# Performance work log

Measured on AMD Instinct MI355X. Metric: run time of the kernel, lower is better.

## Reference

```python
import jax, jax.numpy as jnp
import numpy as np
import math

B, QLEN, KLEN = 8, 128, 1024
KDIM = QDIM = ADIM = ODIM = 512
HM, HC = 4, 4            # monotonic / chunkwise heads
CHUNK = 4                # chunkwise attention window
EPS = 1e-6
SHARPENING = 1.0
NEG_INF = float(np.finfo(np.float32).min)


def moving_sum(x, back, forward):
    """Windowed sum over last axis: out[k] = sum_{j=k-back}^{k+forward} x[j].
    Equivalent to the conv1d-with-ones-filter moving_sum in the torch code."""
    K = x.shape[-1]
    xp = jnp.pad(x, [(0, 0)] * (x.ndim - 1) + [(back, forward)])
    cs = jnp.cumsum(xp, axis=-1)
    L = back + forward + 1
    upper = jax.lax.slice_in_dim(cs, L - 1, L - 1 + K, axis=-1)
    lower = jnp.concatenate([jnp.zeros_like(cs[..., :1]),
                             jax.lax.slice_in_dim(cs, 0, K - 1, axis=-1)], axis=-1)
    return upper - lower


def safe_cumprod(x, eps):
    """exp(exclusive_cumsum(log(clip(x, eps, 1)))) along last axis."""
    logx = jnp.log(jnp.clip(x, eps, 1.0))
    excl = jnp.concatenate([jnp.zeros_like(logx[..., :1]),
                            jnp.cumsum(logx, axis=-1)[..., :-1]], axis=-1)
    return jnp.exp(excl)


def _heads(x, w, b, h):
    y = x @ w + b                                   # [B, L, ADIM]
    bs, L, _ = y.shape
    return y.reshape(bs, L, h, -1).transpose(0, 2, 1, 3)  # [B, h, L, d_k]


def setup_inputs() -> dict:
    key = jax.random.key(0)
    ks = jax.random.split(key, 16)
    s = 0.02
    f32 = jnp.float32
    return {
        "key_x": jax.random.normal(ks[0], (B, KLEN, KDIM), f32),
        "query_x": jax.random.normal(ks[1], (B, QLEN, QDIM), f32),
        "mask": jnp.ones((B, QLEN, KLEN), jnp.int32),
        "wk_m": jax.random.normal(ks[2], (KDIM, ADIM), f32) * s,
        "bk_m": jnp.zeros((ADIM,), f32),
        "wq_m": jax.random.normal(ks[3], (QDIM, ADIM), f32) * s,
        "bq_m": jnp.zeros((ADIM,), f32),
        "r": jnp.asarray(-4.0, f32),
        "wk_c": jax.random.normal(ks[4], (KDIM, ADIM), f32) * s,
        "bk_c": jnp.zeros((ADIM,), f32),
        "wq_c": jax.random.normal(ks[5], (QDIM, ADIM), f32) * s,
        "bq_c": jnp.zeros((ADIM,), f32),
        "wv": jax.random.normal(ks[6], (KDIM, ADIM), f32) * s,
        "bv": jnp.zeros((ADIM,), f32),
        "wo": jax.random.normal(ks[7], (ADIM, ODIM), f32) * s,
        "bo": jnp.zeros((ODIM,), f32),
    }


def reference(key_x, query_x, mask, wk_m, bk_m, wq_m, bq_m, r,
              wk_c, bk_c, wq_c, bq_c, wv, bv, wo, bo):
    scale = math.sqrt(ADIM)
    m = (mask[:, None] > 0)                                    # [B,1,Q,K]

    # ---- monotonic energy (scaled_dot + offset r) ----
    km = _heads(key_x, wk_m, bk_m, HM)                         # [B,HM,K,dk]
    qm = _heads(query_x, wq_m, bq_m, HM)                       # [B,HM,Q,dk]
    e_mono = jnp.einsum('bhqd,bhkd->bhqk', qm, km) / scale + r
    e_mono = jnp.where(m, e_mono, NEG_INF)

    # ---- monotonic alpha via safe_cumprod + per-step cumsum recurrence ----
    p_choose = jax.nn.sigmoid(e_mono)                          # [B,HM,Q,K]
    cp = safe_cumprod(1.0 - p_choose, EPS)                     # [B,HM,Q,K]
    aw0 = jnp.zeros((B, HM, KLEN), e_mono.dtype).at[..., 0].set(1.0)

    def step(aw_prev, pc):
        p_i, cp_i = pc                                         # [B,HM,K]
        aw = p_i * cp_i * jnp.cumsum(aw_prev / jnp.maximum(cp_i, EPS), axis=-1)
        return aw, aw

    _, alpha = jax.lax.scan(step, aw0,
                            (p_choose.transpose(2, 0, 1, 3),
                             cp.transpose(2, 0, 1, 3)))
    alpha = alpha.transpose(1, 2, 0, 3)                        # [B,HM,Q,K]

    # ---- chunkwise energy ----
    kc = _heads(key_x, wk_c, bk_c, HC)
    qc = _heads(query_x, wq_c, bq_c, HC)
    e_chunk = jnp.einsum('bhqd,bhkd->bhqk', qc, kc) / scale
    e_chunk = jnp.where(m, e_chunk, NEG_INF)

    # ---- efficient chunkwise attention (clipped-logit trick) ----
    e = e_chunk - jnp.max(e_chunk, axis=-1, keepdims=True)
    sexp = jnp.maximum(jnp.exp(e), 1e-5)[:, None]              # [B,1,HC,Q,K]
    denom = moving_sum(sexp, CHUNK - 1, 0)                     # [B,1,HC,Q,K]
    beta = sexp * moving_sum(alpha[:, :, None] * SHARPENING / denom,
                             0, CHUNK - 1)                     # [B,HM,HC,Q,K]
    beta = beta.reshape(B, HM * HC, QLEN, KLEN)

    # ---- context + output projection ----
    v = (key_x @ wv + bv).reshape(B, KLEN, HM * HC, ADIM // (HM * HC))
    cv = jnp.einsum('bhqk,bkhd->bqhd', beta, v).reshape(B, QLEN, ADIM)
    return cv @ wo + bo
```

## Files before the change

### kernel.cpp

```cpp
#include <hip/hip_runtime.h>
#include <hip/hip_bf16.h>


#define NEG_INF (-3.402823466e38f)
#define EPS_MOCHA 1e-6f
#define INV_SCALE 0.04419417382415922f

typedef _Float16 half8 __attribute__((ext_vector_type(8)));
typedef _Float16 half4v __attribute__((ext_vector_type(4)));
typedef float f32x4 __attribute__((ext_vector_type(4)));

#define WAITBAR(N) asm volatile("s_waitcnt vmcnt(" #N ") lgkmcnt(0)\n\ts_barrier" ::: "memory")

__device__ __forceinline__ float frcp(float x) { return __builtin_amdgcn_rcpf(x); }

__device__ __forceinline__ float wave_incl_scan(float x)
{
    int v;
    v = __builtin_amdgcn_update_dpp(0, __builtin_bit_cast(int, x), 0x111, 0xF, 0xF, false);
    x += __builtin_bit_cast(float, v);
    v = __builtin_amdgcn_update_dpp(0, __builtin_bit_cast(int, x), 0x112, 0xF, 0xF, false);
    x += __builtin_bit_cast(float, v);
    v = __builtin_amdgcn_update_dpp(0, __builtin_bit_cast(int, x), 0x114, 0xF, 0xF, false);
    x += __builtin_bit_cast(float, v);
    v = __builtin_amdgcn_update_dpp(0, __builtin_bit_cast(int, x), 0x118, 0xF, 0xF, false);
    x += __builtin_bit_cast(float, v);
    v = __builtin_amdgcn_update_dpp(0, __builtin_bit_cast(int, x), 0x142, 0xA, 0xF, false);
    x += __builtin_bit_cast(float, v);
    v = __builtin_amdgcn_update_dpp(0, __builtin_bit_cast(int, x), 0x143, 0xC, 0xF, false);
    x += __builtin_bit_cast(float, v);
    return x;
}

__device__ __forceinline__ half8 cvt8(float4 a, float4 b)
{
    half8 h = {(_Float16)a.x, (_Float16)a.y, (_Float16)a.z, (_Float16)a.w,
               (_Float16)b.x, (_Float16)b.y, (_Float16)b.z, (_Float16)b.w};
    return h;
}

__global__ __launch_bounds__(256) void prep_all(
    const float* __restrict__ wk_m, const float* __restrict__ wk_c,
    const float* __restrict__ wv, const float* __restrict__ wq_m,
    const float* __restrict__ wq_c, const float* __restrict__ wo,
    const float* __restrict__ key_x, const float* __restrict__ query_x,
    _Float16* __restrict__ Wt5, _Float16* __restrict__ Wt_wo,
    _Float16* __restrict__ X16)
{
    __shared__ float T[64][65];
    const int bid = blockIdx.x;
    const int t = threadIdx.x;
    if (bid < 384) {
        const int z = bid >> 6, w = bid & 63;
        const float* W = (z == 0) ? wk_m : (z == 1) ? wk_c : (z == 2) ? wv
                       : (z == 3) ? wq_m : (z == 4) ? wq_c : wo;
        _Float16* O = (z < 5) ? (Wt5 + (size_t)z * 262144) : Wt_wo;
        const int n0 = (w & 7) * 64, k0 = (w >> 3) * 64;
        const int rr = t >> 4, cc = (t & 15) * 4;
#pragma unroll
        for (int r = 0; r < 4; ++r) {
            int k = r * 16 + rr;
            float4 v = *(const float4*)(W + (size_t)(k0 + k) * 512 + n0 + cc);
            T[k][cc + 0] = v.x; T[k][cc + 1] = v.y;
            T[k][cc + 2] = v.z; T[k][cc + 3] = v.w;
        }
        __syncthreads();
        const int nn = t >> 2, kc = (t & 3) * 16;
        _Float16 tmp[16];
#pragma unroll
        for (int i = 0; i < 16; ++i) tmp[i] = (_Float16)T[kc + i][nn];
        _Float16* Op = O + (size_t)(n0 + nn) * 512 + k0 + kc;
        *(half8*)(Op)     = *(half8*)&tmp[0];
        *(half8*)(Op + 8) = *(half8*)&tmp[8];
    } else {
        const size_t KELEMS = (size_t)8192 * 512;
        size_t o = ((size_t)(bid - 384) * 256 + t) * 8;
        const float* s = (o < KELEMS) ? (key_x + o) : (query_x + (o - KELEMS));
        float4 a = *(const float4*)s;
        float4 b = *(const float4*)(s + 4);
        *(half8*)(X16 + o) = cvt8(a, b);
    }
}

__device__ __forceinline__ void stage16(const _Float16* src, _Float16* dst)
{
    __builtin_amdgcn_global_load_lds(
        (const __attribute__((address_space(1))) void*)src,
        (__attribute__((address_space(3))) void*)dst, 16, 0, 0);
}

template <int NSTEPS>
__device__ __forceinline__ void gemm8_f16(
    const _Float16* __restrict__ Abase, const _Float16* __restrict__ Bbase,
    _Float16* As, _Float16* Bs, f32x4 acc[4][2])
{
    const int tid = threadIdx.x;
    const int lane = tid & 63, wave = tid >> 6;
    const int wm = wave >> 2, wn = wave & 3;
    const int col = lane & 15, quad = lane >> 4;
    const int r0 = tid >> 2, seg = tid & 3;

    const _Float16* Ag = Abase + (size_t)r0 * 512 + seg * 8;
    const _Float16* Bg = Bbase + (size_t)r0 * 512 + seg * 8;

    stage16(Ag, As + tid * 8);
    stage16(Bg, Bs + tid * 8);
    if (NSTEPS > 1) {
        stage16(Ag + 32, As + 4096 + tid * 8);
        stage16(Bg + 32, Bs + 4096 + tid * 8);
        WAITBAR(2);
    } else {
        WAITBAR(0);
    }

#pragma unroll
    for (int ks = 0; ks < NSTEPS; ++ks) {
        const int cur = ks % 3;
        if (ks + 2 < NSTEPS) {
            const int s2 = (ks + 2) % 3;
            stage16(Ag + (ks + 2) * 32, As + s2 * 4096 + tid * 8);
            stage16(Bg + (ks + 2) * 32, Bs + s2 * 4096 + tid * 8);
        }
        const _Float16* Afr = As + cur * 4096 + (size_t)(wm * 64 + col) * 32 + quad * 8;
        const _Float16* Bfr = Bs + cur * 4096 + (size_t)(wn * 32 + col) * 32 + quad * 8;
        half8 a[4], b[2];
#pragma unroll
        for (int t = 0; t < 4; ++t) a[t] = *(const half8*)(Afr + (size_t)t * 16 * 32);
#pragma unroll
        for (int t = 0; t < 2; ++t) b[t] = *(const half8*)(Bfr + (size_t)t * 16 * 32);
#pragma unroll
        for (int mt = 0; mt < 4; ++mt)
#pragma unroll
            for (int nt = 0; nt < 2; ++nt)
                acc[mt][nt] = __builtin_amdgcn_mfma_f32_16x16x32_f16(
                    a[mt], b[nt], acc[mt][nt], 0, 0, 0);
        if (ks + 2 < NSTEPS)      WAITBAR(2);
        else if (ks + 1 < NSTEPS) WAITBAR(0);
    }
}

__device__ __forceinline__ void proj_epilogue8(
    f32x4 acc[4][2], const float* __restrict__ bias, void* __restrict__ Cv,
    int m0, int n0, int f16o)
{
    const int tid = threadIdx.x;
    const int lane = tid & 63, wave = tid >> 6;
    const int wm = wave >> 2, wn = wave & 3;
    const int col = lane & 15, quad = lane >> 4;
    float bnt[2];
#pragma unroll
    for (int nt = 0; nt < 2; ++nt)
        bnt[nt] = bias[n0 + wn * 32 + nt * 16 + col];
#pragma unroll
    for (int mt = 0; mt < 4; ++mt) {
        const int rowb = m0 + wm * 64 + mt * 16 + quad * 4;
#pragma unroll
        for (int nt = 0; nt < 2; ++nt) {
            const int cc = n0 + wn * 32 + nt * 16 + col;
#pragma unroll
            for (int r = 0; r < 4; ++r) {
                float v = acc[mt][nt][r] + bnt[nt];
                if (f16o)
                    ((_Float16*)Cv)[(size_t)(rowb + r) * 512 + cc] = (_Float16)v;
                else
                    ((float*)Cv)[(size_t)(rowb + r) * 512 + cc] = v;
            }
        }
    }
}

__global__ __launch_bounds__(512, 8) void mfma_proj5(
    const _Float16* __restrict__ X16, const _Float16* __restrict__ Wt5,
    const float* __restrict__ b0, void* __restrict__ C0,
    const float* __restrict__ b1, void* __restrict__ C1,
    const float* __restrict__ b2, void* __restrict__ C2,
    const float* __restrict__ b3, void* __restrict__ C3,
    const float* __restrict__ b4, void* __restrict__ C4)
{
    __shared__ _Float16 As[12288];
    __shared__ _Float16 Bs[12288];
    const int bid = (blockIdx.x & 7) * 104 + (blockIdx.x >> 3);
    int g, mblk, nblk;
    if (bid < 768) {
        g = bid >> 8; mblk = (bid & 255) >> 2; nblk = bid & 3;
    } else {
        const int t = bid - 768;
        g = 3 + (t >> 5); mblk = (t & 31) >> 2; nblk = t & 3;
    }
    const bool qry = g >= 3;
    const _Float16* A = X16 + (qry ? (size_t)8192 * 512 : 0);
    const _Float16* Wt = Wt5 + (size_t)g * 262144;
    const float* bias = (g == 0) ? b0 : (g == 1) ? b1 : (g == 2) ? b2
                      : (g == 3) ? b3 : b4;
    void* Cv = (g == 0) ? C0 : (g == 1) ? C1 : (g == 2) ? C2
             : (g == 3) ? C3 : C4;
    const int m0 = mblk * 128, n0 = nblk * 128;

    f32x4 acc[4][2];
#pragma unroll
    for (int mt = 0; mt < 4; ++mt)
#pragma unroll
        for (int nt = 0; nt < 2; ++nt) acc[mt][nt] = (f32x4)0.f;
    gemm8_f16<16>(A + (size_t)m0 * 512, Wt + (size_t)n0 * 512, As, Bs, acc);
    proj_epilogue8(acc, bias, Cv, m0, n0, 1);
}

__global__ __launch_bounds__(512, 4) void mfma_proj_out(
    const _Float16* __restrict__ A16, const _Float16* __restrict__ Wt,
    const float* __restrict__ bias, float* __restrict__ C)
{
    __shared__ _Float16 As[12288];
    __shared__ _Float16 Bs[12288];
    const int m0 = blockIdx.x * 128, n0 = blockIdx.y * 128;
    f32x4 acc[4][2];
#pragma unroll
    for (int mt = 0; mt < 4; ++mt)
#pragma unroll
        for (int nt = 0; nt < 2; ++nt) acc[mt][nt] = (f32x4)0.f;
    gemm8_f16<16>(A16 + (size_t)m0 * 512, Wt + (size_t)n0 * 512, As, Bs, acc);
    proj_epilogue8(acc, bias, C, m0, n0, 0);
}

__global__ __launch_bounds__(512, 4) void energy_mfma(
    const _Float16* __restrict__ Qm, const _Float16* __restrict__ Km,
    const _Float16* __restrict__ Qc, const _Float16* __restrict__ Kc,
    const int* __restrict__ mask, float* __restrict__ e_mono,
    _Float16* __restrict__ e_chunk16, const float* __restrict__ r_ptr)
{
    __shared__ _Float16 As[12288];
    __shared__ _Float16 Bs[12288];
    const int tid = threadIdx.x;
    const int lane = tid & 63, wave = tid >> 6;
    const int wm = wave >> 2, wn = wave & 3;
    const int col = lane & 15, quad = lane >> 4;
    const int kt0 = blockIdx.x * 128;
    const int h = blockIdx.y;
    const int b = blockIdx.z;
    const float rv = r_ptr[0];
    const int r0 = tid >> 2, seg = tid & 3;

    const _Float16* Am0 = Qm + (size_t)(b * 128) * 512 + h * 128 + (size_t)r0 * 512 + seg * 8;
    const _Float16* Ac0 = Qc + (size_t)(b * 128) * 512 + h * 128 + (size_t)r0 * 512 + seg * 8;
    const _Float16* Bm0 = Km + (size_t)(b * 1024 + kt0) * 512 + h * 128 + (size_t)r0 * 512 + seg * 8;
    const _Float16* Bc0 = Kc + (size_t)(b * 1024 + kt0) * 512 + h * 128 + (size_t)r0 * 512 + seg * 8;
#define EGA(s) (((s) < 4 ? Am0 : Ac0) + ((s) & 3) * 32)
#define EGB(s) (((s) < 4 ? Bm0 : Bc0) + ((s) & 3) * 32)

    f32x4 accM[4][2], accC[4][2];
#pragma unroll
    for (int mt = 0; mt < 4; ++mt)
#pragma unroll
        for (int nt = 0; nt < 2; ++nt) { accM[mt][nt] = (f32x4)0.f; accC[mt][nt] = (f32x4)0.f; }

#pragma unroll
    for (int s = 0; s < 2; ++s) {
        stage16(EGA(s), As + s * 4096 + tid * 8);
        stage16(EGB(s), Bs + s * 4096 + tid * 8);
    }
    WAITBAR(2);

#pragma unroll
    for (int ks = 0; ks < 8; ++ks) {
        const int cur = ks % 3;
        if (ks + 2 < 8) {
            const int s2 = (ks + 2) % 3;
            stage16(EGA(ks + 2), As + s2 * 4096 + tid * 8);
            stage16(EGB(ks + 2), Bs + s2 * 4096 + tid * 8);
        }
        const _Float16* Afr = As + cur * 4096 + (size_t)(wm * 64 + col) * 32 + quad * 8;
        const _Float16* Bfr = Bs + cur * 4096 + (size_t)(wn * 32 + col) * 32 + quad * 8;
        half8 a[4], bf[2];
#pragma unroll
        for (int t = 0; t < 4; ++t) a[t]  = *(const half8*)(Afr + (size_t)t * 16 * 32);
#pragma unroll
        for (int t = 0; t < 2; ++t) bf[t] = *(const half8*)(Bfr + (size_t)t * 16 * 32);
        if (ks < 4) {
#pragma unroll
            for (int mt = 0; mt < 4; ++mt)
#pragma unroll
                for (int nt = 0; nt < 2; ++nt)
                    accM[mt][nt] = __builtin_amdgcn_mfma_f32_16x16x32_f16(a[mt], bf[nt], accM[mt][nt], 0, 0, 0);
        } else {
#pragma unroll
            for (int mt = 0; mt < 4; ++mt)
#pragma unroll
                for (int nt = 0; nt < 2; ++nt)
                    accC[mt][nt] = __builtin_amdgcn_mfma_f32_16x16x32_f16(a[mt], bf[nt], accC[mt][nt], 0, 0, 0);
        }
        if (ks + 2 < 8)      WAITBAR(2);
        else if (ks + 1 < 8) WAITBAR(0);
    }
#undef EGA
#undef EGB

#pragma unroll
    for (int mt = 0; mt < 4; ++mt) {
        const int qb = wm * 64 + mt * 16 + quad * 4;
#pragma unroll
        for (int nt = 0; nt < 2; ++nt) {
            const int kc = kt0 + wn * 32 + nt * 16 + col;
#pragma unroll
            for (int r = 0; r < 4; ++r) {
                const int q = qb + r;
                const int mv = mask[((size_t)b * 128 + q) * 1024 + kc];
                const size_t oi = (((size_t)b * 4 + h) * 128 + q) * 1024 + kc;
                float vm = accM[mt][nt][r] * INV_SCALE + rv;
                e_mono[oi] = mv ? vm : NEG_INF;
                float vc = accC[mt][nt][r] * INV_SCALE;
                e_chunk16[oi] = (_Float16)(mv ? vc : NEG_INF);
            }
        }
    }
}

__device__ __forceinline__ void transcend_row(
    const float* __restrict__ Erow, int lane, float o_pcp[16], float o_inv[16])
{
    const float* E = Erow + lane * 16;
    float e[16];
    *(float4*)&e[0]  = *(const float4*)(E);
    *(float4*)&e[4]  = *(const float4*)(E + 4);
    *(float4*)&e[8]  = *(const float4*)(E + 8);
    *(float4*)&e[12] = *(const float4*)(E + 12);

    float p[16], l[16];
#pragma unroll
    for (int i = 0; i < 16; ++i) {
        p[i] = frcp(1.f + __expf(-e[i]));
        l[i] = __logf(fmaxf(1.f - p[i], EPS_MOCHA));
    }
    float incl[16];
    incl[0] = l[0];
#pragma unroll
    for (int i = 1; i < 16; ++i) incl[i] = incl[i - 1] + l[i];
    float total = incl[15];
    float x = wave_incl_scan(total);
    float base = x - total;
#pragma unroll
    for (int i = 0; i < 16; ++i) {
        float cl = base + (i ? incl[i - 1] : 0.f);
        float cp = __expf(cl);
        o_pcp[i] = p[i] * cp;
        o_inv[i] = frcp(fmaxf(cp, EPS_MOCHA));
    }
}

#define SW2(k) ((k) + ((k) >> 4))

__global__ __launch_bounds__(512) void alpha_pre(
    const float* __restrict__ e_mono, float* __restrict__ G,
    float* __restrict__ pcp)
{
    __shared__ float pshare[8][1088];
    const int tid = threadIdx.x;
    const int lane = tid & 63;
    const int wid = tid >> 6;
    const int row = blockIdx.x * 8 + wid;
    const int q = row & 127;

    float pq[16], iq[16];
    transcend_row(e_mono + (size_t)row * 1024, lane, pq, iq);

    float* P = pcp + (size_t)row * 1024 + lane * 16;
    *(float4*)(P)      = *(float4*)&pq[0];
    *(float4*)(P + 4)  = *(float4*)&pq[4];
    *(float4*)(P + 8)  = *(float4*)&pq[8];
    *(float4*)(P + 12) = *(float4*)&pq[12];

#pragma unroll
    for (int i = 0; i < 16; ++i)
        pshare[wid][SW2(lane * 16 + i)] = pq[i];
    __syncthreads();

    float g[16];
    if (q == 0) {
#pragma unroll
        for (int i = 0; i < 16; ++i) g[i] = 0.f;
        if (lane == 0) g[0] = iq[0];
    } else if (wid > 0) {
#pragma unroll
        for (int i = 0; i < 16; ++i)
            g[i] = pshare[wid - 1][SW2(lane * 16 + i)] * iq[i];
    } else {
        float pm[16], im[16];
        transcend_row(e_mono + (size_t)(row - 1) * 1024, lane, pm, im);
#pragma unroll
        for (int i = 0; i < 16; ++i) g[i] = pm[i] * iq[i];
    }
    float* Gp = G + (size_t)row * 1024 + lane * 16;
    *(float4*)(Gp)      = *(float4*)&g[0];
    *(float4*)(Gp + 4)  = *(float4*)&g[4];
    *(float4*)(Gp + 8)  = *(float4*)&g[8];
    *(float4*)(Gp + 12) = *(float4*)&g[12];
}

__global__ __launch_bounds__(64, 1) void alpha_scan(
    const float* __restrict__ G, const float* __restrict__ pcp,
    float* __restrict__ alpha)
{
    const int lane = threadIdx.x;
    const int bh = blockIdx.x;
    const float* Gp = G + (size_t)bh * 131072 + lane * 16;
    const float* Pp = pcp + (size_t)bh * 131072 + lane * 16;
    float* Ap = alpha + (size_t)bh * 131072 + lane * 16;

    float bg[8][16], bp[8][16];
#pragma unroll
    for (int s = 0; s < 8; ++s) {
        const float* Gq = Gp + (size_t)s * 1024;
        const float* Pq = Pp + (size_t)s * 1024;
        *(float4*)&bg[s][0]  = *(const float4*)(Gq);
        *(float4*)&bg[s][4]  = *(const float4*)(Gq + 4);
        *(float4*)&bg[s][8]  = *(const float4*)(Gq + 8);
        *(float4*)&bg[s][12] = *(const float4*)(Gq + 12);
        *(float4*)&bp[s][0]  = *(const float4*)(Pq);
        *(float4*)&bp[s][4]  = *(const float4*)(Pq + 4);
        *(float4*)&bp[s][8]  = *(const float4*)(Pq + 8);
        *(float4*)&bp[s][12] = *(const float4*)(Pq + 12);
    }

    float Sv[16];
#pragma unroll
    for (int i = 0; i < 16; ++i) Sv[i] = 1.f;

    for (int q8 = 0; q8 < 128; q8 += 8) {
#pragma unroll
        for (int s = 0; s < 8; ++s) {
            const int q = q8 + s;
            float g[16], pv[16];
#pragma unroll
            for (int i = 0; i < 16; ++i) { g[i] = bg[s][i]; pv[i] = bp[s][i]; }
            if (q + 8 < 128) {
                const float* Gq = Gp + (size_t)(q + 8) * 1024;
                const float* Pq = Pp + (size_t)(q + 8) * 1024;
                *(float4*)&bg[s][0]  = *(const float4*)(Gq);
                *(float4*)&bg[s][4]  = *(const float4*)(Gq + 4);
                *(float4*)&bg[s][8]  = *(const float4*)(Gq + 8);
                *(float4*)&bg[s][12] = *(const float4*)(Gq + 12);
                *(float4*)&bp[s][0]  = *(const float4*)(Pq);
                *(float4*)&bp[s][4]  = *(const float4*)(Pq + 4);
                *(float4*)&bp[s][8]  = *(const float4*)(Pq + 8);
                *(float4*)&bp[s][12] = *(const float4*)(Pq + 12);
            }

            float incl[16];
            incl[0] = g[0] * Sv[0];
#pragma unroll
            for (int i = 1; i < 16; ++i)
                incl[i] = fmaf(g[i], Sv[i], incl[i - 1]);
            float total = incl[15];
            float x = wave_incl_scan(total);
            float base = x - total;
#pragma unroll
            for (int i = 0; i < 16; ++i) Sv[i] = base + incl[i];

            float av[16];
#pragma unroll
            for (int i = 0; i < 16; ++i) av[i] = pv[i] * Sv[i];
            float* Aq = Ap + (size_t)q * 1024;
            *(float4*)(Aq)      = *(float4*)&av[0];
            *(float4*)(Aq + 4)  = *(float4*)&av[4];
            *(float4*)(Aq + 8)  = *(float4*)&av[8];
            *(float4*)(Aq + 12) = *(float4*)&av[12];
        }
    }
}

__global__ __launch_bounds__(256) void beta_kernel(
    const _Float16* __restrict__ e_chunk16, const float* __restrict__ alpha,
    _Float16* __restrict__ beta)
{
    __shared__ float red[4];
    __shared__ float edge_sx[4][4];
    __shared__ float edge_t[4][4][4];
    const int q = blockIdx.x, b = blockIdx.y;
    const int tid = threadIdx.x;
    const int lane = tid & 63, wid = tid >> 6;
    const int k4 = tid * 4;

    float av[4][4];
#pragma unroll
    for (int hm = 0; hm < 4; ++hm) {
        const size_t off = (((size_t)b * 4 + hm) * 128 + q) * 1024 + k4;
        float4 a = *(const float4*)(alpha + off);
        av[hm][0] = a.x; av[hm][1] = a.y; av[hm][2] = a.z; av[hm][3] = a.w;
    }

    for (int hc = 0; hc < 4; ++hc) {
        half4v ev = *(const half4v*)(e_chunk16 + (((size_t)b * 4 + hc) * 128 + q) * 1024 + k4);
        float e[4] = {(float)ev[0], (float)ev[1], (float)ev[2], (float)ev[3]};

        float mx = fmaxf(fmaxf(e[0], e[1]), fmaxf(e[2], e[3]));
#pragma unroll
        for (int off = 32; off >= 1; off >>= 1)
            mx = fmaxf(mx, __shfl_xor(mx, off, 64));
        if (lane == 0) red[wid] = mx;
        __syncthreads();
        mx = fmaxf(fmaxf(red[0], red[1]), fmaxf(red[2], red[3]));

        float sx[4];
#pragma unroll
        for (int i = 0; i < 4; ++i)
            sx[i] = fmaxf(__expf(e[i] - mx), 1e-5f);
        if (lane == 63) {
            edge_sx[wid][0] = sx[0]; edge_sx[wid][1] = sx[1];
            edge_sx[wid][2] = sx[2]; edge_sx[wid][3] = sx[3];
        }
        __syncthreads();

        float p1 = __shfl_up(sx[3], 1, 64);
        float p2 = __shfl_up(sx[2], 1, 64);
        float p3 = __shfl_up(sx[1], 1, 64);
        if (lane == 0) {
            if (wid > 0) {
                p1 = edge_sx[wid - 1][3];
                p2 = edge_sx[wid - 1][2];
                p3 = edge_sx[wid - 1][1];
            } else {
                p1 = 0.f; p2 = 0.f; p3 = 0.f;
            }
        }
        float den[4];
        den[0] = sx[0] + p1 + p2 + p3;
        den[1] = sx[1] + sx[0] + p1 + p2;
        den[2] = sx[2] + sx[1] + sx[0] + p1;
        den[3] = sx[3] + sx[2] + sx[1] + sx[0];
        float rd[4];
#pragma unroll
        for (int i = 0; i < 4; ++i) rd[i] = frcp(den[i]);

        float t[4][4];
#pragma unroll
        for (int hm = 0; hm < 4; ++hm)
#pragma unroll
            for (int i = 0; i < 4; ++i)
                t[hm][i] = av[hm][i] * rd[i];
        if (lane == 0) {
#pragma unroll
            for (int hm = 0; hm < 4; ++hm) {
                edge_t[wid][hm][0] = t[hm][0]; edge_t[wid][hm][1] = t[hm][1];
                edge_t[wid][hm][2] = t[hm][2]; edge_t[wid][hm][3] = t[hm][3];
            }
        }
        __syncthreads();

#pragma unroll
        for (int hm = 0; hm < 4; ++hm) {
            float n1 = __shfl_down(t[hm][0], 1, 64);
            float n2 = __shfl_down(t[hm][1], 1, 64);
            float n3 = __shfl_down(t[hm][2], 1, 64);
            if (lane == 63) {
                if (wid < 3) {
                    n1 = edge_t[wid + 1][hm][0];
                    n2 = edge_t[wid + 1][hm][1];
                    n3 = edge_t[wid + 1][hm][2];
                } else {
                    n1 = 0.f; n2 = 0.f; n3 = 0.f;
                }
            }
            float o0 = sx[0] * (t[hm][0] + t[hm][1] + t[hm][2] + t[hm][3]);
            float o1 = sx[1] * (t[hm][1] + t[hm][2] + t[hm][3] + n1);
            float o2 = sx[2] * (t[hm][2] + t[hm][3] + n1 + n2);
            float o3 = sx[3] * (t[hm][3] + n1 + n2 + n3);
            _Float16* Brow = beta + (((size_t)b * 16 + hm * 4 + hc) * 128 + q) * 1024;
            half4v hv = {(_Float16)o0, (_Float16)o1, (_Float16)o2, (_Float16)o3};
            *(half4v*)(Brow + k4) = hv;
        }
    }
}

__global__ __launch_bounds__(256) void context_kernel(
    const _Float16* __restrict__ beta, const _Float16* __restrict__ V16,
    _Float16* __restrict__ cv16)
{
    __shared__ float bS[128][64];
    __shared__ float vS[128][32];
    const int qh = blockIdx.x, h = blockIdx.y, b = blockIdx.z;
    const int tid = threadIdx.x;
    const int ty = tid >> 3, tx = tid & 7;
    const int q0 = qh * 64;

    const _Float16* Bbase = beta + (((size_t)b * 16 + h) * 128 + q0) * 1024;
    const _Float16* Vbase = V16 + (size_t)b * 1024 * 512 + h * 32;

    float acc[2][4];
#pragma unroll
    for (int i = 0; i < 2; ++i)
#pragma unroll
        for (int j = 0; j < 4; ++j) acc[i][j] = 0.f;

    for (int k0 = 0; k0 < 1024; k0 += 128) {
        {
            int r = tid >> 2, c = tid & 3;
#pragma unroll
            for (int s = 0; s < 4; ++s) {
                half8 v = *(const half8*)(Bbase + (size_t)r * 1024 + k0 + s * 32 + c * 8);
#pragma unroll
                for (int j = 0; j < 8; ++j) bS[s * 32 + c * 8 + j][r] = (float)v[j];
            }
        }
        {
            int kk = tid >> 3, c = tid & 7;
#pragma unroll
            for (int s = 0; s < 4; ++s) {
                half4v v = *(const half4v*)(Vbase + (size_t)(k0 + s * 32 + kk) * 512 + c * 4);
                float4 f = {(float)v[0], (float)v[1], (float)v[2], (float)v[3]};
                *(float4*)&vS[s * 32 + kk][c * 4] = f;
            }
        }
        __syncthreads();
#pragma unroll 8
        for (int kk = 0; kk < 128; ++kk) {
            float a0 = bS[kk][ty * 2], a1 = bS[kk][ty * 2 + 1];
            float bb[4];
            *(float4*)bb = *(const float4*)&vS[kk][tx * 4];
#pragma unroll
            for (int j = 0; j < 4; ++j) {
                acc[0][j] = fmaf(a0, bb[j], acc[0][j]);
                acc[1][j] = fmaf(a1, bb[j], acc[1][j]);
            }
        }
        __syncthreads();
    }
#pragma unroll
    for (int i = 0; i < 2; ++i) {
        _Float16* Cp = cv16 + ((size_t)b * 128 + q0 + ty * 2 + i) * 512 + h * 32 + tx * 4;
        half4v hv = {(_Float16)acc[i][0], (_Float16)acc[i][1],
                     (_Float16)acc[i][2], (_Float16)acc[i][3]};
        *(half4v*)Cp = hv;
    }
}

extern "C" void kernel_launch(void* const* d_in, const int* in_sizes, int n_in,
                              void* d_out, int out_size, void* d_ws, size_t ws_size,
                              hipStream_t stream)
{
    const float* key_x   = (const float*)d_in[0];
    const float* query_x = (const float*)d_in[1];
    const int*   mask    = (const int*)d_in[2];
    const float* wk_m = (const float*)d_in[3];
    const float* bk_m = (const float*)d_in[4];
    const float* wq_m = (const float*)d_in[5];
    const float* bq_m = (const float*)d_in[6];
    const float* r    = (const float*)d_in[7];
    const float* wk_c = (const float*)d_in[8];
    const float* bk_c = (const float*)d_in[9];
    const float* wq_c = (const float*)d_in[10];
    const float* bq_c = (const float*)d_in[11];
    const float* wv   = (const float*)d_in[12];
    const float* bv   = (const float*)d_in[13];
    const float* wo   = (const float*)d_in[14];
    const float* bo   = (const float*)d_in[15];
    float* out = (float*)d_out;

    float* ws = (float*)d_ws;
    _Float16* hws = (_Float16*)d_ws;
    const size_t MEGF = 1024 * 1024;
    _Float16* Km16  = hws;
    _Float16* Kc16  = hws + 4 * MEGF;
    _Float16* Qm16  = hws + 8 * MEGF;
    _Float16* Qc16  = hws + 8 * MEGF + 524288;
    _Float16* X16   = hws + 16 * MEGF;
    float* e_mono  = ws + 11 * MEGF;
    _Float16* e_chunk16 = hws + 34 * MEGF;
    _Float16* V16  = hws + 38 * MEGF;
    float* G       = ws;
    float* pcp     = ws + 4 * MEGF;
    float* alpha   = ws + 23 * MEGF;
    _Float16* beta16 = hws + 16 * MEGF;
    _Float16* Wt5   = hws + 54 * MEGF;
    _Float16* Wt_wo = hws + 54 * MEGF + 5 * 262144;
    _Float16* cv16  = hws + 55 * MEGF + MEGF / 2;

    prep_all<<<dim3(2688), 256, 0, stream>>>(
        wk_m, wk_c, wv, wq_m, wq_c, wo, key_x, query_x, Wt5, Wt_wo, X16);
    mfma_proj5<<<dim3(832), 512, 0, stream>>>(
        X16, Wt5, bk_m, Km16, bk_c, Kc16, bv, V16, bq_m, Qm16, bq_c, Qc16);
    energy_mfma<<<dim3(8, 4, 8), 512, 0, stream>>>(
        Qm16, Km16, Qc16, Kc16, mask, e_mono, e_chunk16, r);
    alpha_pre<<<dim3(512), 512, 0, stream>>>(e_mono, G, pcp);
    alpha_scan<<<dim3(32), 64, 0, stream>>>(G, pcp, alpha);
    beta_kernel<<<dim3(128, 8), 256, 0, stream>>>(e_chunk16, alpha, beta16);
    context_kernel<<<dim3(2, 16, 8), 256, 0, stream>>>(beta16, V16, cv16);
    mfma_proj_out<<<dim3(8, 4), 512, 0, stream>>>(cv16, Wt_wo, bo, out);
}
```

Before: 255.8 us.

## Split alpha scan across four waves with LDS carry exchange per row

The alpha_scan kernel now uses 256 threads per (batch, head) block instead of a single wave. Each thread owns 4 keys instead of 16, and wave totals are combined through a double-buffered shared-memory carry with a barrier every query step. This shortens each thread's serial inner chain and spreads the loads over more lanes. The cost is 128 block barriers and some LDS traffic per block, and the grid stays at only 32 blocks.

```diff
diff --git a/kernel.cpp b/kernel.cpp
--- a/kernel.cpp
+++ b/kernel.cpp
@@ -11,6 +11,7 @@
 typedef float f32x4 __attribute__((ext_vector_type(4)));
 
 #define WAITBAR(N) asm volatile("s_waitcnt vmcnt(" #N ") lgkmcnt(0)\n\ts_barrier" ::: "memory")
+#define BARLG() asm volatile("s_waitcnt lgkmcnt(0)\n\ts_barrier" ::: "memory")
 
 __device__ __forceinline__ float frcp(float x) { return __builtin_amdgcn_rcpf(x); }
 
@@ -394,75 +395,54 @@
     *(float4*)(Gp + 12) = *(float4*)&g[12];
 }
 
-__global__ __launch_bounds__(64, 1) void alpha_scan(
+__global__ __launch_bounds__(256) void alpha_scan(
     const float* __restrict__ G, const float* __restrict__ pcp,
     float* __restrict__ alpha)
 {
-    const int lane = threadIdx.x;
+    __shared__ float carry[2][4];
+    const int tid = threadIdx.x;
+    const int lane = tid & 63, wid = tid >> 6;
     const int bh = blockIdx.x;
-    const float* Gp = G + (size_t)bh * 131072 + lane * 16;
-    const float* Pp = pcp + (size_t)bh * 131072 + lane * 16;
-    float* Ap = alpha + (size_t)bh * 131072 + lane * 16;
-
-    float bg[8][16], bp[8][16];
-#pragma unroll
-    for (int s = 0; s < 8; ++s) {
-        const float* Gq = Gp + (size_t)s * 1024;
-        const float* Pq = Pp + (size_t)s * 1024;
-        *(float4*)&bg[s][0]  = *(const float4*)(Gq);
-        *(float4*)&bg[s][4]  = *(const float4*)(Gq + 4);
-        *(float4*)&bg[s][8]  = *(const float4*)(Gq + 8);
-        *(float4*)&bg[s][12] = *(const float4*)(Gq + 12);
-        *(float4*)&bp[s][0]  = *(const float4*)(Pq);
-        *(float4*)&bp[s][4]  = *(const float4*)(Pq + 4);
-        *(float4*)&bp[s][8]  = *(const float4*)(Pq + 8);
-        *(float4*)&bp[s][12] = *(const float4*)(Pq + 12);
-    }
-
-    float Sv[16];
-#pragma unroll
-    for (int i = 0; i < 16; ++i) Sv[i] = 1.f;
-
-    for (int q8 = 0; q8 < 128; q8 += 8) {
-#pragma unroll
-        for (int s = 0; s < 8; ++s) {
-            const int q = q8 + s;
-            float g[16], pv[16];
-#pragma unroll
-            for (int i = 0; i < 16; ++i) { g[i] = bg[s][i]; pv[i] = bp[s][i]; }
-            if (q + 8 < 128) {
-                const float* Gq = Gp + (size_t)(q + 8) * 1024;
-                const float* Pq = Pp + (size_t)(q + 8) * 1024;
-                *(float4*)&bg[s][0]  = *(const float4*)(Gq);
-                *(float4*)&bg[s][4]  = *(const float4*)(Gq + 4);
-                *(float4*)&bg[s][8]  = *(const float4*)(Gq + 8);
-                *(float4*)&bg[s][12] = *(const float4*)(Gq + 12);
-                *(float4*)&bp[s][0]  = *(const float4*)(Pq);
-                *(float4*)&bp[s][4]  = *(const float4*)(Pq + 4);
-                *(float4*)&bp[s][8]  = *(const float4*)(Pq + 8);
-                *(float4*)&bp[s][12] = *(const float4*)(Pq + 12);
-            }
-
-            float incl[16];
-            incl[0] = g[0] * Sv[0];
-#pragma unroll
-            for (int i = 1; i < 16; ++i)
-                incl[i] = fmaf(g[i], Sv[i], incl[i - 1]);
-            float total = incl[15];
-            float x = wave_incl_scan(total);
-            float base = x - total;
-#pragma unroll
-            for (int i = 0; i < 16; ++i) Sv[i] = base + incl[i];
-
-            float av[16];
-#pragma unroll
-            for (int i = 0; i < 16; ++i) av[i] = pv[i] * Sv[i];
-            float* Aq = Ap + (size_t)q * 1024;
-            *(float4*)(Aq)      = *(float4*)&av[0];
-            *(float4*)(Aq + 4)  = *(float4*)&av[4];
-            *(float4*)(Aq + 8)  = *(float4*)&av[8];
-            *(float4*)(Aq + 12) = *(float4*)&av[12];
-        }
+    const float* Gp = G + (size_t)bh * 131072 + tid * 4;
+    const float* Pp = pcp + (size_t)bh * 131072 + tid * 4;
+    float* Ap = alpha + (size_t)bh * 131072 + tid * 4;
+
+    float4 bg[4], bp[4];
+#pragma unroll
+    for (int s = 0; s < 4; ++s) {
+        bg[s] = *(const float4*)(Gp + (size_t)s * 1024);
+        bp[s] = *(const float4*)(Pp + (size_t)s * 1024);
+    }
+
+    float Sv[4] = {1.f, 1.f, 1.f, 1.f};
+
+    for (int q = 0; q < 128; ++q) {
+        const int s = q & 3;
+        float g[4] = {bg[s].x, bg[s].y, bg[s].z, bg[s].w};
+        float p[4] = {bp[s].x, bp[s].y, bp[s].z, bp[s].w};
+        if (q + 4 < 128) {
+            bg[s] = *(const float4*)(Gp + (size_t)(q + 4) * 1024);
+            bp[s] = *(const float4*)(Pp + (size_t)(q + 4) * 1024);
+        }
+        float incl[4];
+        incl[0] = g[0] * Sv[0];
+        incl[1] = fmaf(g[1], Sv[1], incl[0]);
+        incl[2] = fmaf(g[2], Sv[2], incl[1]);
+        incl[3] = fmaf(g[3], Sv[3], incl[2]);
+        float t = incl[3];
+        float x = wave_incl_scan(t);
+        float base = x - t;
+        if (lane == 63) carry[q & 1][wid] = x;
+        BARLG();
+        float pre = 0.f;
+        if (wid > 0) pre += carry[q & 1][0];
+        if (wid > 1) pre += carry[q & 1][1];
+        if (wid > 2) pre += carry[q & 1][2];
+        float baseAll = pre + base;
+#pragma unroll
+        for (int i = 0; i < 4; ++i) Sv[i] = baseAll + incl[i];
+        float4 av = {p[0] * Sv[0], p[1] * Sv[1], p[2] * Sv[2], p[3] * Sv[3]};
+        *(float4*)(Ap + (size_t)q * 1024) = av;
     }
 }
 
@@ -679,7 +659,7 @@
     energy_mfma<<<dim3(8, 4, 8), 512, 0, stream>>>(
         Qm16, Km16, Qc16, Kc16, mask, e_mono, e_chunk16, r);
     alpha_pre<<<dim3(512), 512, 0, stream>>>(e_mono, G, pcp);
-    alpha_scan<<<dim3(32), 64, 0, stream>>>(G, pcp, alpha);
+    alpha_scan<<<dim3(32), 256, 0, stream>>>(G, pcp, alpha);
     beta_kernel<<<dim3(128, 8), 256, 0, stream>>>(e_chunk16, alpha, beta16);
     context_kernel<<<dim3(2, 16, 8), 256, 0, stream>>>(beta16, V16, cv16);
     mfma_proj_out<<<dim3(8, 4), 512, 0, stream>>>(cv16, Wt_wo, bo, out);
```

New measurement: 293.2 us. +14.6%, slower.
